# Performance work log

Measured on AMD Instinct MI355X. Metric: run time of the kernel, lower is better.

Reference implementation:

```python
import jax, jax.numpy as jnp
import numpy as np

EMBED = 1024
HIDDEN = 64  # embed_size // n_heads
B, L = 8, 4096


def setup_inputs() -> dict:
    key = jax.random.key(0)
    k1, k2, k3, k4, k5, k6, k7 = jax.random.split(key, 7)
    query = jax.random.normal(k1, (B, L, EMBED), dtype=jnp.float32)
    key_t = jax.random.normal(k2, (B, L, EMBED), dtype=jnp.float32)
    value = jax.random.normal(k3, (B, L, EMBED), dtype=jnp.float32)
    mask = jax.random.randint(k4, (B, L, L), 0, 2).astype(jnp.bool_)
    # nn.Linear(embed, hidden, bias=False) weights have shape (hidden, embed)
    s = 1.0 / np.sqrt(EMBED)
    WQ = jax.random.uniform(k5, (HIDDEN, EMBED), jnp.float32, -s, s)
    WK = jax.random.uniform(k6, (HIDDEN, EMBED), jnp.float32, -s, s)
    WV = jax.random.uniform(k7, (HIDDEN, EMBED), jnp.float32, -s, s)
    return {"query": query, "key": key_t, "value": value, "mask": mask,
            "WQ": WQ, "WK": WK, "WV": WV}


def reference(query, key, value, mask, WQ, WK, WV):
    # Projections: y = x @ W.T  (Linear without bias)
    Q = jnp.einsum('ble,he->blh', query, WQ)   # [B,L,H]
    K = jnp.einsum('ble,he->blh', key, WK)
    V = jnp.einsum('ble,he->blh', value, WV)
    scale = 1.0 / jnp.sqrt(jnp.asarray(Q.shape[-1], Q.dtype))
    scores = jnp.einsum('bqh,bkh->bqk', Q, K) * scale   # [B,L,L]
    scores = jnp.where(mask, -jnp.inf, scores)
    attn = jax.nn.softmax(scores, axis=-1)
    # dropout p=0.0 -> identity
    return jnp.einsum('bqk,bkh->bqh', attn, V)           # [B,L,H]
```

## Files before the change

kernel.cpp:

```cpp
#include <hip/hip_runtime.h>
#include <hip/hip_bf16.h>

#define NB 8
#define LL 4096
#define EE 1024
#define HH 64

typedef unsigned short u16;
typedef unsigned char u8;
typedef unsigned int u32;
typedef unsigned long long u64;
using bf16x8 = __attribute__((ext_vector_type(8))) short;
using f32x4  = __attribute__((ext_vector_type(4))) float;

__device__ __forceinline__ short f2bf(float f) {
    __hip_bfloat16 h = __float2bfloat16(f);
    return __builtin_bit_cast(short, h);
}

__device__ __forceinline__ bf16x8 pack8(const float4 a, const float4 b) {
    bf16x8 r;
    r[0] = f2bf(a.x); r[1] = f2bf(a.y); r[2] = f2bf(a.z); r[3] = f2bf(a.w);
    r[4] = f2bf(b.x); r[5] = f2bf(b.y); r[6] = f2bf(b.z); r[7] = f2bf(b.w);
    return r;
}

__global__ __launch_bounds__(256) void proj_kernel(
    const float* __restrict__ Xq, const float* __restrict__ Xk, const float* __restrict__ Xv,
    const float* __restrict__ Wq, const float* __restrict__ Wk, const float* __restrict__ Wv,
    u16* __restrict__ Oq, u16* __restrict__ Ok, u16* __restrict__ Ovt)
{
    __shared__ u16 Xs[2][64][72];
    __shared__ u16 Ws2[2][64][72];

    const int which = blockIdx.y;
    const float* X = (which == 0) ? Xq : (which == 1) ? Xk : Xv;
    const float* W = (which == 0) ? Wq : (which == 1) ? Wk : Wv;
    const float scale = (which == 0) ? 0.125f : 1.0f;

    const int tid  = threadIdx.x;
    const int lane = tid & 63;
    const int w    = tid >> 6;
    const int g    = lane >> 4;
    const int c    = lane & 15;
    const int m0   = blockIdx.x * 64;
    const int r    = tid >> 2;
    const int cb   = (tid & 3) * 16;

    const float* xrow = X + (size_t)(m0 + r) * EE + cb;
    const float* wrow = W + (size_t)r * EE + cb;

    float4 xr[4], wr[4];
    #pragma unroll
    for (int i = 0; i < 4; ++i) {
        xr[i] = reinterpret_cast<const float4*>(xrow)[i];
        wr[i] = reinterpret_cast<const float4*>(wrow)[i];
    }
    *reinterpret_cast<bf16x8*>(&Xs[0][r][cb])      = pack8(xr[0], xr[1]);
    *reinterpret_cast<bf16x8*>(&Xs[0][r][cb + 8])  = pack8(xr[2], xr[3]);
    *reinterpret_cast<bf16x8*>(&Ws2[0][r][cb])     = pack8(wr[0], wr[1]);
    *reinterpret_cast<bf16x8*>(&Ws2[0][r][cb + 8]) = pack8(wr[2], wr[3]);
    __syncthreads();

    f32x4 acc[4];
    #pragma unroll
    for (int t = 0; t < 4; ++t) acc[t] = (f32x4){0.f, 0.f, 0.f, 0.f};

    for (int s = 0; s < 16; ++s) {
        const int curb = s & 1, nxtb = curb ^ 1;
        if (s < 15) {
            #pragma unroll
            for (int i = 0; i < 4; ++i) {
                xr[i] = reinterpret_cast<const float4*>(xrow + (s + 1) * 64)[i];
                wr[i] = reinterpret_cast<const float4*>(wrow + (s + 1) * 64)[i];
            }
        }
        __builtin_amdgcn_s_setprio(1);
        #pragma unroll
        for (int kk = 0; kk < 2; ++kk) {
            bf16x8 a = *reinterpret_cast<const bf16x8*>(&Xs[curb][16*w + c][kk*32 + 8*g]);
            #pragma unroll
            for (int t = 0; t < 4; ++t) {
                bf16x8 bb = *reinterpret_cast<const bf16x8*>(&Ws2[curb][16*t + c][kk*32 + 8*g]);
                acc[t] = __builtin_amdgcn_mfma_f32_16x16x32_bf16(a, bb, acc[t], 0, 0, 0);
            }
        }
        __builtin_amdgcn_s_setprio(0);
        if (s < 15) {
            *reinterpret_cast<bf16x8*>(&Xs[nxtb][r][cb])      = pack8(xr[0], xr[1]);
            *reinterpret_cast<bf16x8*>(&Xs[nxtb][r][cb + 8])  = pack8(xr[2], xr[3]);
            *reinterpret_cast<bf16x8*>(&Ws2[nxtb][r][cb])     = pack8(wr[0], wr[1]);
            *reinterpret_cast<bf16x8*>(&Ws2[nxtb][r][cb + 8]) = pack8(wr[2], wr[3]);
        }
        __syncthreads();
    }

    if (which < 2) {
        u16* O = (which == 0) ? Oq : Ok;
        #pragma unroll
        for (int t = 0; t < 4; ++t)
            #pragma unroll
            for (int q = 0; q < 4; ++q) {
                const int mrow = m0 + 16*w + 4*g + q;
                O[(size_t)mrow * HH + 16*t + c] = (u16)f2bf(acc[t][q] * scale);
            }
    } else {
        const int bidx = m0 >> 12;
        #pragma unroll
        for (int t = 0; t < 4; ++t)
            #pragma unroll
            for (int q = 0; q < 4; ++q) {
                const int l = (m0 & (LL - 1)) + 16*w + 4*g + q;
                Ovt[((size_t)bidx * HH + 16*t + c) * LL + l] = (u16)f2bf(acc[t][q]);
            }
    }
}

__global__ __launch_bounds__(256) void attn_kernel(
    const u16* __restrict__ Qb, const u16* __restrict__ Kb, const u16* __restrict__ Vt,
    const int* __restrict__ mask, float* __restrict__ out)
{
    __shared__ u16 Ks[2][64][72];
    __shared__ u16 Vts[2][64][72];
    __shared__ u64 Mb[2][64];
    __shared__ u16 Ps[4][16][72];

    const int b    = blockIdx.y;
    const int q0   = blockIdx.x * 64;
    const int tid  = threadIdx.x;
    const int lane = tid & 63;
    const int w    = tid >> 6;
    const int g    = lane >> 4;
    const int c    = lane & 15;
    const int r    = tid >> 2;
    const int cb   = (tid & 3) * 16;

    const u16* kbase = Kb + (size_t)b * LL * HH;
    const u16* vbase = Vt + (size_t)b * HH * LL;
    const int* mbase = mask + (size_t)b * LL * LL + (size_t)(q0 + r) * LL + cb;

    bf16x8 qf[2];
    {
        const u16* qp = Qb + ((size_t)b * LL + q0 + 16*w + c) * HH;
        qf[0] = *reinterpret_cast<const bf16x8*>(qp + 8*g);
        qf[1] = *reinterpret_cast<const bf16x8*>(qp + 32 + 8*g);
    }

    u32 mA[16], mB[16];
    #define LOADM(dst, kt_) do {                                               \
        const int4* _p = reinterpret_cast<const int4*>(mbase + (kt_) * 64);    \
        _Pragma("unroll")                                                      \
        for (int _i = 0; _i < 4; ++_i) {                                       \
            int4 _v = _p[_i];                                                  \
            dst[4*_i+0] = (u32)_v.x; dst[4*_i+1] = (u32)_v.y;                  \
            dst[4*_i+2] = (u32)_v.z; dst[4*_i+3] = (u32)_v.w;                  \
        }                                                                      \
    } while (0)
    #define PACKM(buf_, src) do {                                              \
        u32 _bits = 0;                                                         \
        _Pragma("unroll")                                                      \
        for (int _i = 0; _i < 16; ++_i) _bits |= (u32)(src[_i] != 0) << _i;    \
        ((u16*)&Mb[buf_][r])[tid & 3] = (u16)_bits;                            \
    } while (0)

    bf16x8 kra = *reinterpret_cast<const bf16x8*>(kbase + (size_t)r * HH + cb);
    bf16x8 krb = *reinterpret_cast<const bf16x8*>(kbase + (size_t)r * HH + cb + 8);
    bf16x8 vra = *reinterpret_cast<const bf16x8*>(vbase + (size_t)r * LL + cb);
    bf16x8 vrb = *reinterpret_cast<const bf16x8*>(vbase + (size_t)r * LL + cb + 8);
    LOADM(mB, 0);
    LOADM(mA, 1);
    *reinterpret_cast<bf16x8*>(&Ks[0][r][cb])      = kra;
    *reinterpret_cast<bf16x8*>(&Ks[0][r][cb + 8])  = krb;
    *reinterpret_cast<bf16x8*>(&Vts[0][r][cb])     = vra;
    *reinterpret_cast<bf16x8*>(&Vts[0][r][cb + 8]) = vrb;
    PACKM(0, mB);
    __syncthreads();

    f32x4 acc[4];
    float lpart[4];
    #pragma unroll
    for (int t = 0; t < 4; ++t) acc[t] = (f32x4){0.f, 0.f, 0.f, 0.f};
    #pragma unroll
    for (int q = 0; q < 4; ++q) lpart[q] = 0.f;

    #define TILE_BODY(CUR) do {                                                \
        f32x4 s[4];                                                            \
        __builtin_amdgcn_s_setprio(1);                                         \
        _Pragma("unroll")                                                      \
        for (int t = 0; t < 4; ++t) {                                          \
            s[t] = (f32x4){0.f, 0.f, 0.f, 0.f};                                \
            _Pragma("unroll")                                                  \
            for (int kk = 0; kk < 2; ++kk) {                                   \
                bf16x8 bfr = *reinterpret_cast<const bf16x8*>(&Ks[CUR][16*t + c][kk*32 + 8*g]); \
                s[t] = __builtin_amdgcn_mfma_f32_16x16x32_bf16(qf[kk], bfr, s[t], 0, 0, 0);     \
            }                                                                  \
        }                                                                      \
        __builtin_amdgcn_s_setprio(0);                                         \
        u32 mlo[4], mhi[4];                                                    \
        _Pragma("unroll")                                                      \
        for (int q = 0; q < 4; ++q) {                                          \
            u64 mwq = Mb[CUR][16*w + 4*g + q];                                 \
            mlo[q] = (u32)mwq; mhi[q] = (u32)(mwq >> 32);                      \
        }                                                                      \
        _Pragma("unroll")                                                      \
        for (int t = 0; t < 4; ++t)                                            \
            _Pragma("unroll")                                                  \
            for (int q = 0; q < 4; ++q) {                                      \
                u32 wsel = (t < 2) ? mlo[q] : mhi[q];                          \
                u32 bit = (wsel >> ((t & 1) * 16 + c)) & 1u;                   \
                float p = bit ? 0.f : __expf(s[t][q]);                         \
                lpart[q] += p;                                                 \
                Ps[w][4*g + q][16*t + c] = (u16)f2bf(p);                       \
            }                                                                  \
        __builtin_amdgcn_s_setprio(1);                                         \
        _Pragma("unroll")                                                      \
        for (int kk = 0; kk < 2; ++kk) {                                       \
            bf16x8 pa = *reinterpret_cast<const bf16x8*>(&Ps[w][c][kk*32 + 8*g]);               \
            _Pragma("unroll")                                                  \
            for (int t = 0; t < 4; ++t) {                                      \
                bf16x8 vfr = *reinterpret_cast<const bf16x8*>(&Vts[CUR][16*t + c][kk*32 + 8*g]);\
                acc[t] = __builtin_amdgcn_mfma_f32_16x16x32_bf16(pa, vfr, acc[t], 0, 0, 0);     \
            }                                                                  \
        }                                                                      \
        __builtin_amdgcn_s_setprio(0);                                         \
    } while (0)

    #define LOADKV(kt_) do {                                                   \
        kra = *reinterpret_cast<const bf16x8*>(kbase + (size_t)((kt_)*64 + r) * HH + cb);       \
        krb = *reinterpret_cast<const bf16x8*>(kbase + (size_t)((kt_)*64 + r) * HH + cb + 8);   \
        vra = *reinterpret_cast<const bf16x8*>(vbase + (size_t)r * LL + (kt_)*64 + cb);         \
        vrb = *reinterpret_cast<const bf16x8*>(vbase + (size_t)r * LL + (kt_)*64 + cb + 8);     \
    } while (0)
    #define WRITEKV(buf_) do {                                                 \
        *reinterpret_cast<bf16x8*>(&Ks[buf_][r][cb])      = kra;               \
        *reinterpret_cast<bf16x8*>(&Ks[buf_][r][cb + 8])  = krb;               \
        *reinterpret_cast<bf16x8*>(&Vts[buf_][r][cb])     = vra;               \
        *reinterpret_cast<bf16x8*>(&Vts[buf_][r][cb + 8]) = vrb;               \
    } while (0)

    for (int kt = 0; kt < LL / 64; kt += 2) {
        if (kt + 2 < LL / 64) LOADM(mB, kt + 2);
        LOADKV(kt + 1);
        TILE_BODY(0);
        WRITEKV(1);
        PACKM(1, mA);
        __syncthreads();

        if (kt + 2 < LL / 64) {
            if (kt + 3 < LL / 64) LOADM(mA, kt + 3);
            LOADKV(kt + 2);
        }
        TILE_BODY(1);
        if (kt + 2 < LL / 64) {
            WRITEKV(0);
            PACKM(0, mB);
        }
        __syncthreads();
    }

    #pragma unroll
    for (int off = 8; off >= 1; off >>= 1)
        #pragma unroll
        for (int q = 0; q < 4; ++q)
            lpart[q] += __shfl_xor(lpart[q], off, 64);
    #pragma unroll
    for (int q = 0; q < 4; ++q) {
        const float inv = 1.0f / lpart[q];
        const size_t row = (size_t)b * LL + q0 + 16*w + 4*g + q;
        #pragma unroll
        for (int t = 0; t < 4; ++t)
            out[row * HH + 16*t + c] = acc[t][q] * inv;
    }
}

extern "C" void kernel_launch(void* const* d_in, const int* in_sizes, int n_in,
                              void* d_out, int out_size, void* d_ws, size_t ws_size,
                              hipStream_t stream) {
    const float* query = (const float*)d_in[0];
    const float* key_t = (const float*)d_in[1];
    const float* value = (const float*)d_in[2];
    const int*   mask  = (const int*)d_in[3];
    const float* WQ    = (const float*)d_in[4];
    const float* WK    = (const float*)d_in[5];
    const float* WV    = (const float*)d_in[6];
    float* out = (float*)d_out;

    u16* Qb  = (u16*)d_ws;
    u16* Kb  = Qb + (size_t)NB * LL * HH;
    u16* Vtb = Kb + (size_t)NB * LL * HH;

    dim3 pgrid(NB * LL / 64, 3);
    proj_kernel<<<pgrid, 256, 0, stream>>>(query, key_t, value, WQ, WK, WV, Qb, Kb, Vtb);

    dim3 agrid(LL / 64, NB);
    attn_kernel<<<agrid, 256, 0, stream>>>(Qb, Kb, Vtb, mask, out);
}
```

Before: 236.2 us.

## Split attention key range across two blocks with a combine kernel

Templates the attention kernel on a key-split factor and, when the workspace is large enough, launches twice as many blocks, each covering half of the key tiles. Each block writes unnormalized partial accumulators and row sums to the workspace, and a new elementwise combine kernel adds the two halves and normalizes. The intent is more blocks in flight for better occupancy across the GPU's compute units. The cost is an extra launch plus partial-result global traffic. Since softmax uses no running max, the plain sum combine is exact.

```diff
diff --git a/kernel.cpp b/kernel.cpp
--- a/kernel.cpp
+++ b/kernel.cpp
@@ -116,9 +116,11 @@
     }
 }
 
+template<int NSPLIT>
 __global__ __launch_bounds__(256) void attn_kernel(
     const u16* __restrict__ Qb, const u16* __restrict__ Kb, const u16* __restrict__ Vt,
-    const int* __restrict__ mask, float* __restrict__ out)
+    const int* __restrict__ mask, float* __restrict__ out,
+    float* __restrict__ accp, float* __restrict__ lp)
 {
     __shared__ u16 Ks[2][64][72];
     __shared__ u16 Vts[2][64][72];
@@ -127,6 +129,9 @@
 
     const int b    = blockIdx.y;
     const int q0   = blockIdx.x * 64;
+    const int hf   = (NSPLIT == 2) ? blockIdx.z : 0;
+    const int NTL  = (LL / 64) / NSPLIT;
+    const int kt0  = hf * NTL;
     const int tid  = threadIdx.x;
     const int lane = tid & 63;
     const int w    = tid >> 6;
@@ -147,6 +152,7 @@
     }
 
     u32 mA[16], mB[16];
+    bf16x8 kra, krb, vra, vrb;
     #define LOADM(dst, kt_) do {                                               \
         const int4* _p = reinterpret_cast<const int4*>(mbase + (kt_) * 64);    \
         _Pragma("unroll")                                                      \
@@ -162,19 +168,18 @@
         for (int _i = 0; _i < 16; ++_i) _bits |= (u32)(src[_i] != 0) << _i;    \
         ((u16*)&Mb[buf_][r])[tid & 3] = (u16)_bits;                            \
     } while (0)
-
-    bf16x8 kra = *reinterpret_cast<const bf16x8*>(kbase + (size_t)r * HH + cb);
-    bf16x8 krb = *reinterpret_cast<const bf16x8*>(kbase + (size_t)r * HH + cb + 8);
-    bf16x8 vra = *reinterpret_cast<const bf16x8*>(vbase + (size_t)r * LL + cb);
-    bf16x8 vrb = *reinterpret_cast<const bf16x8*>(vbase + (size_t)r * LL + cb + 8);
-    LOADM(mB, 0);
-    LOADM(mA, 1);
-    *reinterpret_cast<bf16x8*>(&Ks[0][r][cb])      = kra;
-    *reinterpret_cast<bf16x8*>(&Ks[0][r][cb + 8])  = krb;
-    *reinterpret_cast<bf16x8*>(&Vts[0][r][cb])     = vra;
-    *reinterpret_cast<bf16x8*>(&Vts[0][r][cb + 8]) = vrb;
-    PACKM(0, mB);
-    __syncthreads();
+    #define LOADKV(kt_) do {                                                   \
+        kra = *reinterpret_cast<const bf16x8*>(kbase + (size_t)((kt_)*64 + r) * HH + cb);       \
+        krb = *reinterpret_cast<const bf16x8*>(kbase + (size_t)((kt_)*64 + r) * HH + cb + 8);   \
+        vra = *reinterpret_cast<const bf16x8*>(vbase + (size_t)r * LL + (kt_)*64 + cb);         \
+        vrb = *reinterpret_cast<const bf16x8*>(vbase + (size_t)r * LL + (kt_)*64 + cb + 8);     \
+    } while (0)
+    #define WRITEKV(buf_) do {                                                 \
+        *reinterpret_cast<bf16x8*>(&Ks[buf_][r][cb])      = kra;               \
+        *reinterpret_cast<bf16x8*>(&Ks[buf_][r][cb + 8])  = krb;               \
+        *reinterpret_cast<bf16x8*>(&Vts[buf_][r][cb])     = vra;               \
+        *reinterpret_cast<bf16x8*>(&Vts[buf_][r][cb + 8]) = vrb;               \
+    } while (0)
 
     f32x4 acc[4];
     float lpart[4];
@@ -225,33 +230,28 @@
         __builtin_amdgcn_s_setprio(0);                                         \
     } while (0)
 
-    #define LOADKV(kt_) do {                                                   \
-        kra = *reinterpret_cast<const bf16x8*>(kbase + (size_t)((kt_)*64 + r) * HH + cb);       \
-        krb = *reinterpret_cast<const bf16x8*>(kbase + (size_t)((kt_)*64 + r) * HH + cb + 8);   \
-        vra = *reinterpret_cast<const bf16x8*>(vbase + (size_t)r * LL + (kt_)*64 + cb);         \
-        vrb = *reinterpret_cast<const bf16x8*>(vbase + (size_t)r * LL + (kt_)*64 + cb + 8);     \
-    } while (0)
-    #define WRITEKV(buf_) do {                                                 \
-        *reinterpret_cast<bf16x8*>(&Ks[buf_][r][cb])      = kra;               \
-        *reinterpret_cast<bf16x8*>(&Ks[buf_][r][cb + 8])  = krb;               \
-        *reinterpret_cast<bf16x8*>(&Vts[buf_][r][cb])     = vra;               \
-        *reinterpret_cast<bf16x8*>(&Vts[buf_][r][cb + 8]) = vrb;               \
-    } while (0)
-
-    for (int kt = 0; kt < LL / 64; kt += 2) {
-        if (kt + 2 < LL / 64) LOADM(mB, kt + 2);
-        LOADKV(kt + 1);
+    LOADKV(kt0);
+    LOADM(mB, kt0);
+    LOADM(mA, kt0 + 1);
+    WRITEKV(0);
+    PACKM(0, mB);
+    __syncthreads();
+
+    for (int j = 0; j < NTL; j += 2) {
+        const int a = kt0 + j;
+        LOADKV(a + 1);
+        if (j + 2 < NTL) LOADM(mB, a + 2);
         TILE_BODY(0);
         WRITEKV(1);
         PACKM(1, mA);
         __syncthreads();
 
-        if (kt + 2 < LL / 64) {
-            if (kt + 3 < LL / 64) LOADM(mA, kt + 3);
-            LOADKV(kt + 2);
+        if (j + 2 < NTL) {
+            LOADKV(a + 2);
+            if (j + 3 < NTL) LOADM(mA, a + 3);
         }
         TILE_BODY(1);
-        if (kt + 2 < LL / 64) {
+        if (j + 2 < NTL) {
             WRITEKV(0);
             PACKM(0, mB);
         }
@@ -263,14 +263,39 @@
         #pragma unroll
         for (int q = 0; q < 4; ++q)
             lpart[q] += __shfl_xor(lpart[q], off, 64);
-    #pragma unroll
-    for (int q = 0; q < 4; ++q) {
-        const float inv = 1.0f / lpart[q];
-        const size_t row = (size_t)b * LL + q0 + 16*w + 4*g + q;
-        #pragma unroll
-        for (int t = 0; t < 4; ++t)
-            out[row * HH + 16*t + c] = acc[t][q] * inv;
-    }
+
+    if constexpr (NSPLIT == 1) {
+        #pragma unroll
+        for (int q = 0; q < 4; ++q) {
+            const float inv = 1.0f / lpart[q];
+            const size_t row = (size_t)b * LL + q0 + 16*w + 4*g + q;
+            #pragma unroll
+            for (int t = 0; t < 4; ++t)
+                out[row * HH + 16*t + c] = acc[t][q] * inv;
+        }
+    } else {
+        float* acch = accp + (size_t)hf * NB * LL * HH;
+        float* lph  = lp + (size_t)hf * NB * LL;
+        #pragma unroll
+        for (int q = 0; q < 4; ++q) {
+            const size_t row = (size_t)b * LL + q0 + 16*w + 4*g + q;
+            #pragma unroll
+            for (int t = 0; t < 4; ++t)
+                acch[row * HH + 16*t + c] = acc[t][q];
+            if (c == 0) lph[row] = lpart[q];
+        }
+    }
+}
+
+__global__ __launch_bounds__(256) void combine_kernel(
+    const float* __restrict__ accp, const float* __restrict__ lp,
+    float* __restrict__ out)
+{
+    const size_t N = (size_t)NB * LL * HH;
+    const size_t idx = (size_t)blockIdx.x * 256 + threadIdx.x;
+    const size_t row = idx >> 6;
+    float l = lp[row] + lp[(size_t)NB * LL + row];
+    out[idx] = (accp[idx] + accp[N + idx]) / l;
 }
 
 extern "C" void kernel_launch(void* const* d_in, const int* in_sizes, int n_in,
@@ -285,13 +310,23 @@
     const float* WV    = (const float*)d_in[6];
     float* out = (float*)d_out;
 
+    const size_t nqkv = (size_t)NB * LL * HH;
     u16* Qb  = (u16*)d_ws;
-    u16* Kb  = Qb + (size_t)NB * LL * HH;
-    u16* Vtb = Kb + (size_t)NB * LL * HH;
+    u16* Kb  = Qb + nqkv;
+    u16* Vtb = Kb + nqkv;
+    float* accp = (float*)(Vtb + nqkv);
+    float* lp   = accp + 2 * nqkv;
+    const size_t need_split = (3 * nqkv) * 2 + 2 * nqkv * 4 + 2 * (size_t)NB * LL * 4;
 
     dim3 pgrid(NB * LL / 64, 3);
     proj_kernel<<<pgrid, 256, 0, stream>>>(query, key_t, value, WQ, WK, WV, Qb, Kb, Vtb);
 
-    dim3 agrid(LL / 64, NB);
-    attn_kernel<<<agrid, 256, 0, stream>>>(Qb, Kb, Vtb, mask, out);
-}
+    if (ws_size >= need_split) {
+        dim3 agrid(LL / 64, NB, 2);
+        attn_kernel<2><<<agrid, 256, 0, stream>>>(Qb, Kb, Vtb, mask, out, accp, lp);
+        combine_kernel<<<(unsigned)(nqkv / 256), 256, 0, stream>>>(accp, lp, out);
+    } else {
+        dim3 agrid(LL / 64, NB, 1);
+        attn_kernel<1><<<agrid, 256, 0, stream>>>(Qb, Kb, Vtb, mask, out, nullptr, nullptr);
+    }
+}
```

New measurement: 238.4 us. No clear change (+0.9%).

## Precompute packed mask bits in projection kernel and read them directly in attention

Applied to the files above, without the earlier changes.

Moves mask-to-bitmask packing out of the attention kernel into a grid-stride tail of the projection kernel, which writes a packed u16-per-16-elements bit array to workspace. The attention kernel then loads 64-bit mask words per row straight from global memory into registers, removing the shared-memory mask buffer and its packing work. The full int32 mask is still read once, but the packing now runs in the projection kernel rather than being interleaved with attention compute. It also adds a launch_bounds occupancy hint to the projection kernel and uses extra workspace for the bits.

```diff
diff --git a/kernel.cpp b/kernel.cpp
--- a/kernel.cpp
+++ b/kernel.cpp
@@ -25,9 +25,10 @@
     return r;
 }
 
-__global__ __launch_bounds__(256) void proj_kernel(
+__global__ __launch_bounds__(256, 4) void proj_kernel(
     const float* __restrict__ Xq, const float* __restrict__ Xk, const float* __restrict__ Xv,
     const float* __restrict__ Wq, const float* __restrict__ Wk, const float* __restrict__ Wv,
+    const int* __restrict__ mask, u16* __restrict__ bitsOut,
     u16* __restrict__ Oq, u16* __restrict__ Ok, u16* __restrict__ Ovt)
 {
     __shared__ u16 Xs[2][64][72];
@@ -114,15 +115,31 @@
                 Ovt[((size_t)bidx * HH + 16*t + c) * LL + l] = (u16)f2bf(acc[t][q]);
             }
     }
+
+    const size_t NW = (size_t)NB * LL * LL / 16;
+    const size_t wstride = (size_t)gridDim.x * 3 * 256;
+    size_t wi = ((size_t)blockIdx.y * gridDim.x + blockIdx.x) * 256 + tid;
+    for (; wi < NW; wi += wstride) {
+        const int4* p = reinterpret_cast<const int4*>(mask + wi * 16);
+        int4 v0 = p[0], v1 = p[1], v2 = p[2], v3 = p[3];
+        u32 bits =  (u32)(v0.x != 0)        | ((u32)(v0.y != 0) << 1)
+                 | ((u32)(v0.z != 0) << 2)  | ((u32)(v0.w != 0) << 3)
+                 | ((u32)(v1.x != 0) << 4)  | ((u32)(v1.y != 0) << 5)
+                 | ((u32)(v1.z != 0) << 6)  | ((u32)(v1.w != 0) << 7)
+                 | ((u32)(v2.x != 0) << 8)  | ((u32)(v2.y != 0) << 9)
+                 | ((u32)(v2.z != 0) << 10) | ((u32)(v2.w != 0) << 11)
+                 | ((u32)(v3.x != 0) << 12) | ((u32)(v3.y != 0) << 13)
+                 | ((u32)(v3.z != 0) << 14) | ((u32)(v3.w != 0) << 15);
+        bitsOut[wi] = (u16)bits;
+    }
 }
 
 __global__ __launch_bounds__(256) void attn_kernel(
     const u16* __restrict__ Qb, const u16* __restrict__ Kb, const u16* __restrict__ Vt,
-    const int* __restrict__ mask, float* __restrict__ out)
+    const u64* __restrict__ mbits, float* __restrict__ out)
 {
     __shared__ u16 Ks[2][64][72];
     __shared__ u16 Vts[2][64][72];
-    __shared__ u64 Mb[2][64];
     __shared__ u16 Ps[4][16][72];
 
     const int b    = blockIdx.y;
@@ -137,7 +154,7 @@
 
     const u16* kbase = Kb + (size_t)b * LL * HH;
     const u16* vbase = Vt + (size_t)b * HH * LL;
-    const int* mbase = mask + (size_t)b * LL * LL + (size_t)(q0 + r) * LL + cb;
+    const u64* mbp = mbits + (size_t)(b * LL + q0 + 16*w + 4*g) * 64;
 
     bf16x8 qf[2];
     {
@@ -146,35 +163,24 @@
         qf[1] = *reinterpret_cast<const bf16x8*>(qp + 32 + 8*g);
     }
 
-    u32 mA[16], mB[16];
-    #define LOADM(dst, kt_) do {                                               \
-        const int4* _p = reinterpret_cast<const int4*>(mbase + (kt_) * 64);    \
-        _Pragma("unroll")                                                      \
-        for (int _i = 0; _i < 4; ++_i) {                                       \
-            int4 _v = _p[_i];                                                  \
-            dst[4*_i+0] = (u32)_v.x; dst[4*_i+1] = (u32)_v.y;                  \
-            dst[4*_i+2] = (u32)_v.z; dst[4*_i+3] = (u32)_v.w;                  \
-        }                                                                      \
-    } while (0)
-    #define PACKM(buf_, src) do {                                              \
-        u32 _bits = 0;                                                         \
-        _Pragma("unroll")                                                      \
-        for (int _i = 0; _i < 16; ++_i) _bits |= (u32)(src[_i] != 0) << _i;    \
-        ((u16*)&Mb[buf_][r])[tid & 3] = (u16)_bits;                            \
-    } while (0)
-
-    bf16x8 kra = *reinterpret_cast<const bf16x8*>(kbase + (size_t)r * HH + cb);
-    bf16x8 krb = *reinterpret_cast<const bf16x8*>(kbase + (size_t)r * HH + cb + 8);
-    bf16x8 vra = *reinterpret_cast<const bf16x8*>(vbase + (size_t)r * LL + cb);
-    bf16x8 vrb = *reinterpret_cast<const bf16x8*>(vbase + (size_t)r * LL + cb + 8);
-    LOADM(mB, 0);
-    LOADM(mA, 1);
-    *reinterpret_cast<bf16x8*>(&Ks[0][r][cb])      = kra;
-    *reinterpret_cast<bf16x8*>(&Ks[0][r][cb + 8])  = krb;
-    *reinterpret_cast<bf16x8*>(&Vts[0][r][cb])     = vra;
-    *reinterpret_cast<bf16x8*>(&Vts[0][r][cb + 8]) = vrb;
-    PACKM(0, mB);
-    __syncthreads();
+    bf16x8 kra, krb, vra, vrb;
+    u64 ma0, ma1, ma2, ma3, mb0, mb1, mb2, mb3;
+    #define LOADKV(kt_) do {                                                   \
+        kra = *reinterpret_cast<const bf16x8*>(kbase + (size_t)((kt_)*64 + r) * HH + cb);       \
+        krb = *reinterpret_cast<const bf16x8*>(kbase + (size_t)((kt_)*64 + r) * HH + cb + 8);   \
+        vra = *reinterpret_cast<const bf16x8*>(vbase + (size_t)r * LL + (kt_)*64 + cb);         \
+        vrb = *reinterpret_cast<const bf16x8*>(vbase + (size_t)r * LL + (kt_)*64 + cb + 8);     \
+    } while (0)
+    #define WRITEKV(buf_) do {                                                 \
+        *reinterpret_cast<bf16x8*>(&Ks[buf_][r][cb])      = kra;               \
+        *reinterpret_cast<bf16x8*>(&Ks[buf_][r][cb + 8])  = krb;               \
+        *reinterpret_cast<bf16x8*>(&Vts[buf_][r][cb])     = vra;               \
+        *reinterpret_cast<bf16x8*>(&Vts[buf_][r][cb + 8]) = vrb;               \
+    } while (0)
+    #define LOADMB(s0, s1, s2, s3, kt_) do {                                   \
+        s0 = mbp[(kt_)]; s1 = mbp[64 + (kt_)];                                 \
+        s2 = mbp[128 + (kt_)]; s3 = mbp[192 + (kt_)];                          \
+    } while (0)
 
     f32x4 acc[4];
     float lpart[4];
@@ -183,7 +189,7 @@
     #pragma unroll
     for (int q = 0; q < 4; ++q) lpart[q] = 0.f;
 
-    #define TILE_BODY(CUR) do {                                                \
+    #define TILE_BODY(CUR, M0, M1, M2, M3) do {                                \
         f32x4 s[4];                                                            \
         __builtin_amdgcn_s_setprio(1);                                         \
         _Pragma("unroll")                                                      \
@@ -197,11 +203,10 @@
         }                                                                      \
         __builtin_amdgcn_s_setprio(0);                                         \
         u32 mlo[4], mhi[4];                                                    \
-        _Pragma("unroll")                                                      \
-        for (int q = 0; q < 4; ++q) {                                          \
-            u64 mwq = Mb[CUR][16*w + 4*g + q];                                 \
-            mlo[q] = (u32)mwq; mhi[q] = (u32)(mwq >> 32);                      \
-        }                                                                      \
+        mlo[0] = (u32)(M0); mhi[0] = (u32)((M0) >> 32);                        \
+        mlo[1] = (u32)(M1); mhi[1] = (u32)((M1) >> 32);                        \
+        mlo[2] = (u32)(M2); mhi[2] = (u32)((M2) >> 32);                        \
+        mlo[3] = (u32)(M3); mhi[3] = (u32)((M3) >> 32);                        \
         _Pragma("unroll")                                                      \
         for (int t = 0; t < 4; ++t)                                            \
             _Pragma("unroll")                                                  \
@@ -225,36 +230,24 @@
         __builtin_amdgcn_s_setprio(0);                                         \
     } while (0)
 
-    #define LOADKV(kt_) do {                                                   \
-        kra = *reinterpret_cast<const bf16x8*>(kbase + (size_t)((kt_)*64 + r) * HH + cb);       \
-        krb = *reinterpret_cast<const bf16x8*>(kbase + (size_t)((kt_)*64 + r) * HH + cb + 8);   \
-        vra = *reinterpret_cast<const bf16x8*>(vbase + (size_t)r * LL + (kt_)*64 + cb);         \
-        vrb = *reinterpret_cast<const bf16x8*>(vbase + (size_t)r * LL + (kt_)*64 + cb + 8);     \
-    } while (0)
-    #define WRITEKV(buf_) do {                                                 \
-        *reinterpret_cast<bf16x8*>(&Ks[buf_][r][cb])      = kra;               \
-        *reinterpret_cast<bf16x8*>(&Ks[buf_][r][cb + 8])  = krb;               \
-        *reinterpret_cast<bf16x8*>(&Vts[buf_][r][cb])     = vra;               \
-        *reinterpret_cast<bf16x8*>(&Vts[buf_][r][cb + 8]) = vrb;               \
-    } while (0)
+    LOADKV(0);
+    LOADMB(ma0, ma1, ma2, ma3, 0);
+    WRITEKV(0);
+    __syncthreads();
 
     for (int kt = 0; kt < LL / 64; kt += 2) {
-        if (kt + 2 < LL / 64) LOADM(mB, kt + 2);
         LOADKV(kt + 1);
-        TILE_BODY(0);
+        LOADMB(mb0, mb1, mb2, mb3, kt + 1);
+        TILE_BODY(0, ma0, ma1, ma2, ma3);
         WRITEKV(1);
-        PACKM(1, mA);
         __syncthreads();
 
         if (kt + 2 < LL / 64) {
-            if (kt + 3 < LL / 64) LOADM(mA, kt + 3);
             LOADKV(kt + 2);
-        }
-        TILE_BODY(1);
-        if (kt + 2 < LL / 64) {
-            WRITEKV(0);
-            PACKM(0, mB);
-        }
+            LOADMB(ma0, ma1, ma2, ma3, kt + 2);
+        }
+        TILE_BODY(1, mb0, mb1, mb2, mb3);
+        if (kt + 2 < LL / 64) WRITEKV(0);
         __syncthreads();
     }
 
@@ -285,13 +278,16 @@
     const float* WV    = (const float*)d_in[6];
     float* out = (float*)d_out;
 
-    u16* Qb  = (u16*)d_ws;
-    u16* Kb  = Qb + (size_t)NB * LL * HH;
-    u16* Vtb = Kb + (size_t)NB * LL * HH;
+    const size_t nqkv = (size_t)NB * LL * HH;
+    u16* Qb   = (u16*)d_ws;
+    u16* Kb   = Qb + nqkv;
+    u16* Vtb  = Kb + nqkv;
+    u16* bits = Vtb + nqkv;
 
     dim3 pgrid(NB * LL / 64, 3);
-    proj_kernel<<<pgrid, 256, 0, stream>>>(query, key_t, value, WQ, WK, WV, Qb, Kb, Vtb);
+    proj_kernel<<<pgrid, 256, 0, stream>>>(query, key_t, value, WQ, WK, WV,
+                                           mask, bits, Qb, Kb, Vtb);
 
     dim3 agrid(LL / 64, NB);
-    attn_kernel<<<agrid, 256, 0, stream>>>(Qb, Kb, Vtb, mask, out);
-}
+    attn_kernel<<<agrid, 256, 0, stream>>>(Qb, Kb, Vtb, (const u64*)bits, out);
+}
```

Measured after the change: 294.4 us. 1.25x slower.

## Prefetch mask for four key tiles at once with contiguous per-thread row loads

Applied to the files above, without the earlier changes.

The mask prefetch is restructured so that each thread loads 1KB of contiguous mask ints from one row per four-tile super-step, instead of 64 bytes per tile. The four threads of a row each cover a different tile, and the packed 64-bit bitmaps are double-buffered per super-step in a new shared array. The goal is longer, better-coalesced DRAM bursts on the mask stream, which is the largest memory cost, and fewer mask packing and sync points. In exchange, 16 int4 registers stay live across four tiles, which may raise VGPR pressure and lower occupancy.

```diff
diff --git a/kernel.cpp b/kernel.cpp
--- a/kernel.cpp
+++ b/kernel.cpp
@@ -122,8 +122,8 @@
 {
     __shared__ u16 Ks[2][64][72];
     __shared__ u16 Vts[2][64][72];
-    __shared__ u64 Mb[2][64];
     __shared__ u16 Ps[4][16][72];
+    __shared__ u64 Pnl[2][4][64];
 
     const int b    = blockIdx.y;
     const int q0   = blockIdx.x * 64;
@@ -133,11 +133,12 @@
     const int g    = lane >> 4;
     const int c    = lane & 15;
     const int r    = tid >> 2;
-    const int cb   = (tid & 3) * 16;
+    const int qq   = tid & 3;
+    const int cb   = qq * 16;
 
     const u16* kbase = Kb + (size_t)b * LL * HH;
     const u16* vbase = Vt + (size_t)b * HH * LL;
-    const int* mbase = mask + (size_t)b * LL * LL + (size_t)(q0 + r) * LL + cb;
+    const int* mrowp = mask + (size_t)b * LL * LL + (size_t)(q0 + r) * LL;
 
     bf16x8 qf[2];
     {
@@ -146,35 +147,44 @@
         qf[1] = *reinterpret_cast<const bf16x8*>(qp + 32 + 8*g);
     }
 
-    u32 mA[16], mB[16];
-    #define LOADM(dst, kt_) do {                                               \
-        const int4* _p = reinterpret_cast<const int4*>(mbase + (kt_) * 64);    \
-        _Pragma("unroll")                                                      \
-        for (int _i = 0; _i < 4; ++_i) {                                       \
-            int4 _v = _p[_i];                                                  \
-            dst[4*_i+0] = (u32)_v.x; dst[4*_i+1] = (u32)_v.y;                  \
-            dst[4*_i+2] = (u32)_v.z; dst[4*_i+3] = (u32)_v.w;                  \
+    bf16x8 kra, krb, vra, vrb;
+    int4 sm[16];
+
+    #define LOADKV(kt_) do {                                                   \
+        kra = *reinterpret_cast<const bf16x8*>(kbase + (size_t)((kt_)*64 + r) * HH + cb);       \
+        krb = *reinterpret_cast<const bf16x8*>(kbase + (size_t)((kt_)*64 + r) * HH + cb + 8);   \
+        vra = *reinterpret_cast<const bf16x8*>(vbase + (size_t)r * LL + (kt_)*64 + cb);         \
+        vrb = *reinterpret_cast<const bf16x8*>(vbase + (size_t)r * LL + (kt_)*64 + cb + 8);     \
+    } while (0)
+    #define WRITEKV(buf_) do {                                                 \
+        *reinterpret_cast<bf16x8*>(&Ks[buf_][r][cb])      = kra;               \
+        *reinterpret_cast<bf16x8*>(&Ks[buf_][r][cb + 8])  = krb;               \
+        *reinterpret_cast<bf16x8*>(&Vts[buf_][r][cb])     = vra;               \
+        *reinterpret_cast<bf16x8*>(&Vts[buf_][r][cb + 8]) = vrb;               \
+    } while (0)
+    #define SLOADM(j_) do {                                                    \
+        const int4* _mp = reinterpret_cast<const int4*>(mrowp + ((j_)*4 + qq) * 64); \
+        _Pragma("unroll")                                                      \
+        for (int _i = 0; _i < 16; ++_i) sm[_i] = _mp[_i];                      \
+    } while (0)
+    #define SPACK(buf_) do {                                                   \
+        u32 _lo = 0, _hi = 0;                                                  \
+        _Pragma("unroll")                                                      \
+        for (int _i = 0; _i < 8; ++_i) {                                       \
+            _lo |= ((u32)(sm[_i].x != 0) << (4*_i))                            \
+                |  ((u32)(sm[_i].y != 0) << (4*_i + 1))                        \
+                |  ((u32)(sm[_i].z != 0) << (4*_i + 2))                        \
+                |  ((u32)(sm[_i].w != 0) << (4*_i + 3));                       \
         }                                                                      \
-    } while (0)
-    #define PACKM(buf_, src) do {                                              \
-        u32 _bits = 0;                                                         \
-        _Pragma("unroll")                                                      \
-        for (int _i = 0; _i < 16; ++_i) _bits |= (u32)(src[_i] != 0) << _i;    \
-        ((u16*)&Mb[buf_][r])[tid & 3] = (u16)_bits;                            \
-    } while (0)
-
-    bf16x8 kra = *reinterpret_cast<const bf16x8*>(kbase + (size_t)r * HH + cb);
-    bf16x8 krb = *reinterpret_cast<const bf16x8*>(kbase + (size_t)r * HH + cb + 8);
-    bf16x8 vra = *reinterpret_cast<const bf16x8*>(vbase + (size_t)r * LL + cb);
-    bf16x8 vrb = *reinterpret_cast<const bf16x8*>(vbase + (size_t)r * LL + cb + 8);
-    LOADM(mB, 0);
-    LOADM(mA, 1);
-    *reinterpret_cast<bf16x8*>(&Ks[0][r][cb])      = kra;
-    *reinterpret_cast<bf16x8*>(&Ks[0][r][cb + 8])  = krb;
-    *reinterpret_cast<bf16x8*>(&Vts[0][r][cb])     = vra;
-    *reinterpret_cast<bf16x8*>(&Vts[0][r][cb + 8]) = vrb;
-    PACKM(0, mB);
-    __syncthreads();
+        _Pragma("unroll")                                                      \
+        for (int _i = 8; _i < 16; ++_i) {                                      \
+            _hi |= ((u32)(sm[_i].x != 0) << (4*_i - 32))                       \
+                |  ((u32)(sm[_i].y != 0) << (4*_i - 31))                       \
+                |  ((u32)(sm[_i].z != 0) << (4*_i - 30))                       \
+                |  ((u32)(sm[_i].w != 0) << (4*_i - 29));                      \
+        }                                                                      \
+        Pnl[buf_][qq][r] = ((u64)_hi << 32) | _lo;                             \
+    } while (0)
 
     f32x4 acc[4];
     float lpart[4];
@@ -183,7 +193,7 @@
     #pragma unroll
     for (int q = 0; q < 4; ++q) lpart[q] = 0.f;
 
-    #define TILE_BODY(CUR) do {                                                \
+    #define TILE_BODY(KVB, PB, TI) do {                                        \
         f32x4 s[4];                                                            \
         __builtin_amdgcn_s_setprio(1);                                         \
         _Pragma("unroll")                                                      \
@@ -191,17 +201,20 @@
             s[t] = (f32x4){0.f, 0.f, 0.f, 0.f};                                \
             _Pragma("unroll")                                                  \
             for (int kk = 0; kk < 2; ++kk) {                                   \
-                bf16x8 bfr = *reinterpret_cast<const bf16x8*>(&Ks[CUR][16*t + c][kk*32 + 8*g]); \
+                bf16x8 bfr = *reinterpret_cast<const bf16x8*>(&Ks[KVB][16*t + c][kk*32 + 8*g]); \
                 s[t] = __builtin_amdgcn_mfma_f32_16x16x32_bf16(qf[kk], bfr, s[t], 0, 0, 0);     \
             }                                                                  \
         }                                                                      \
         __builtin_amdgcn_s_setprio(0);                                         \
+        u64 mw0 = Pnl[PB][TI][16*w + 4*g + 0];                                 \
+        u64 mw1 = Pnl[PB][TI][16*w + 4*g + 1];                                 \
+        u64 mw2 = Pnl[PB][TI][16*w + 4*g + 2];                                 \
+        u64 mw3 = Pnl[PB][TI][16*w + 4*g + 3];                                 \
         u32 mlo[4], mhi[4];                                                    \
-        _Pragma("unroll")                                                      \
-        for (int q = 0; q < 4; ++q) {                                          \
-            u64 mwq = Mb[CUR][16*w + 4*g + q];                                 \
-            mlo[q] = (u32)mwq; mhi[q] = (u32)(mwq >> 32);                      \
-        }                                                                      \
+        mlo[0] = (u32)mw0; mhi[0] = (u32)(mw0 >> 32);                          \
+        mlo[1] = (u32)mw1; mhi[1] = (u32)(mw1 >> 32);                          \
+        mlo[2] = (u32)mw2; mhi[2] = (u32)(mw2 >> 32);                          \
+        mlo[3] = (u32)mw3; mhi[3] = (u32)(mw3 >> 32);                          \
         _Pragma("unroll")                                                      \
         for (int t = 0; t < 4; ++t)                                            \
             _Pragma("unroll")                                                  \
@@ -218,42 +231,45 @@
             bf16x8 pa = *reinterpret_cast<const bf16x8*>(&Ps[w][c][kk*32 + 8*g]);               \
             _Pragma("unroll")                                                  \
             for (int t = 0; t < 4; ++t) {                                      \
-                bf16x8 vfr = *reinterpret_cast<const bf16x8*>(&Vts[CUR][16*t + c][kk*32 + 8*g]);\
+                bf16x8 vfr = *reinterpret_cast<const bf16x8*>(&Vts[KVB][16*t + c][kk*32 + 8*g]);\
                 acc[t] = __builtin_amdgcn_mfma_f32_16x16x32_bf16(pa, vfr, acc[t], 0, 0, 0);     \
             }                                                                  \
         }                                                                      \
         __builtin_amdgcn_s_setprio(0);                                         \
     } while (0)
 
-    #define LOADKV(kt_) do {                                                   \
-        kra = *reinterpret_cast<const bf16x8*>(kbase + (size_t)((kt_)*64 + r) * HH + cb);       \
-        krb = *reinterpret_cast<const bf16x8*>(kbase + (size_t)((kt_)*64 + r) * HH + cb + 8);   \
-        vra = *reinterpret_cast<const bf16x8*>(vbase + (size_t)r * LL + (kt_)*64 + cb);         \
-        vrb = *reinterpret_cast<const bf16x8*>(vbase + (size_t)r * LL + (kt_)*64 + cb + 8);     \
-    } while (0)
-    #define WRITEKV(buf_) do {                                                 \
-        *reinterpret_cast<bf16x8*>(&Ks[buf_][r][cb])      = kra;               \
-        *reinterpret_cast<bf16x8*>(&Ks[buf_][r][cb + 8])  = krb;               \
-        *reinterpret_cast<bf16x8*>(&Vts[buf_][r][cb])     = vra;               \
-        *reinterpret_cast<bf16x8*>(&Vts[buf_][r][cb + 8]) = vrb;               \
-    } while (0)
-
-    for (int kt = 0; kt < LL / 64; kt += 2) {
-        if (kt + 2 < LL / 64) LOADM(mB, kt + 2);
-        LOADKV(kt + 1);
-        TILE_BODY(0);
+    LOADKV(0);
+    SLOADM(0);
+    WRITEKV(0);
+    SPACK(0);
+    __syncthreads();
+
+    for (int j = 0; j < 16; ++j) {
+        const int base = 4 * j;
+        const int cur = j & 1, nxt = cur ^ 1;
+        const bool morem = (j + 1 < 16);
+
+        LOADKV(base + 1);
+        if (morem) SLOADM(j + 1);
+        TILE_BODY(0, cur, 0);
         WRITEKV(1);
-        PACKM(1, mA);
-        __syncthreads();
-
-        if (kt + 2 < LL / 64) {
-            if (kt + 3 < LL / 64) LOADM(mA, kt + 3);
-            LOADKV(kt + 2);
-        }
-        TILE_BODY(1);
-        if (kt + 2 < LL / 64) {
+        __syncthreads();
+
+        LOADKV(base + 2);
+        TILE_BODY(1, cur, 1);
+        WRITEKV(0);
+        __syncthreads();
+
+        LOADKV(base + 3);
+        TILE_BODY(0, cur, 2);
+        WRITEKV(1);
+        __syncthreads();
+
+        if (morem) LOADKV(base + 4);
+        TILE_BODY(1, cur, 3);
+        if (morem) {
             WRITEKV(0);
-            PACKM(0, mB);
+            SPACK(nxt);
         }
         __syncthreads();
     }
@@ -285,9 +301,10 @@
     const float* WV    = (const float*)d_in[6];
     float* out = (float*)d_out;
 
+    const size_t nqkv = (size_t)NB * LL * HH;
     u16* Qb  = (u16*)d_ws;
-    u16* Kb  = Qb + (size_t)NB * LL * HH;
-    u16* Vtb = Kb + (size_t)NB * LL * HH;
+    u16* Kb  = Qb + nqkv;
+    u16* Vtb = Kb + nqkv;
 
     dim3 pgrid(NB * LL / 64, 3);
     proj_kernel<<<pgrid, 256, 0, stream>>>(query, key_t, value, WQ, WK, WV, Qb, Kb, Vtb);
```

Measured after the change: 306.2 us. 29.7% more time.
